# Kernel optimization log

Measured on AMD Instinct MI355X. Metric: run time of the kernel, lower is better.

Reference implementation:

```python
import jax, jax.numpy as jnp
import numpy as np
from jax import lax

B, H, W, CIN = 4, 64, 64, 1024
CMID = 512
NA = 9  # 3 sizes * 3 ratios
PRE_NMS, POST_NMS, IOU_THR = 6000, 300, 0.7  # eval-mode caps (training=False)


def setup_inputs() -> dict:
    key = jax.random.key(0)
    ks = jax.random.split(key, 4)
    feats = jax.random.normal(ks[0], (B, H, W, CIN), jnp.float32)
    # anchors: normalized ccwh (cx, cy, w, h) on a stride-16 grid of a 1024px image
    stride, img = 16.0, 1024.0
    cx = (jnp.arange(W, dtype=jnp.float32) + 0.5) * stride / img
    cy = (jnp.arange(H, dtype=jnp.float32) + 0.5) * stride / img
    sizes = jnp.array([64.0, 128.0, 256.0])
    ratios = jnp.array([0.5, 1.0, 2.0])
    ws = (sizes[:, None] * jnp.sqrt(ratios)[None, :]).reshape(-1) / img  # [9]
    hs = (sizes[:, None] / jnp.sqrt(ratios)[None, :]).reshape(-1) / img  # [9]
    cyg, cxg = jnp.meshgrid(cy, cx, indexing='ij')  # [H,W]
    ancs = jnp.stack([
        jnp.broadcast_to(cxg[:, :, None], (H, W, NA)),
        jnp.broadcast_to(cyg[:, :, None], (H, W, NA)),
        jnp.broadcast_to(ws[None, None, :], (H, W, NA)),
        jnp.broadcast_to(hs[None, None, :], (H, W, NA)),
    ], axis=-1)
    ancs = jnp.broadcast_to(ancs[None], (B, H, W, NA, 4)).astype(jnp.float32)
    ancs_valid = jnp.ones((B, H, W, NA), jnp.float32)
    w_bneck = jax.random.normal(ks[1], (CIN, CMID), jnp.float32) * 0.01
    b_bneck = jnp.zeros((CMID,), jnp.float32)
    w_cls = jax.random.normal(ks[2], (CMID, NA), jnp.float32) * 0.01
    b_cls = jnp.zeros((NA,), jnp.float32)
    w_reg = jax.random.normal(ks[3], (CMID, NA * 4), jnp.float32) * 0.01
    b_reg = jnp.zeros((NA * 4,), jnp.float32)
    return dict(feats=feats, ancs=ancs, ancs_valid=ancs_valid,
                w_bneck=w_bneck, b_bneck=b_bneck, w_cls=w_cls, b_cls=b_cls,
                w_reg=w_reg, b_reg=b_reg)


def _nms(boxes, max_out, thr):
    # boxes [N,4] xyxy, sorted by score descending. Greedy NMS via lax.scan.
    x1, y1, x2, y2 = boxes[:, 0], boxes[:, 1], boxes[:, 2], boxes[:, 3]
    areas = (x2 - x1) * (y2 - y1)

    def step(valid, _):
        idx = jnp.argmax(valid)  # first still-valid box = highest score
        has = valid[idx]
        b = boxes[idx]
        a = areas[idx]
        iw = jnp.maximum(jnp.minimum(b[2], x2) - jnp.maximum(b[0], x1), 0.0)
        ih = jnp.maximum(jnp.minimum(b[3], y2) - jnp.maximum(b[1], y1), 0.0)
        inter = iw * ih
        union = a + areas - inter
        iou = jnp.where(union > 0, inter / union, 0.0)
        keep = valid & (iou <= thr)
        keep = keep.at[idx].set(False)
        return jnp.where(has, keep, valid), jnp.where(has, idx, -1)

    _, sel = lax.scan(step, jnp.ones(boxes.shape[0], bool), None, length=max_out)
    return sel  # [max_out] selected indices, -1 = no more boxes


def _forward(feats, ancs, w_bneck, b_bneck, w_cls, b_cls, w_reg, b_reg):
    h = jax.nn.relu(jnp.einsum('bhwc,cm->bhwm', feats, w_bneck) + b_bneck)
    cls_pred = jax.nn.sigmoid(jnp.einsum('bhwm,mo->bhwo', h, w_cls) + b_cls)
    reg_pred = (jnp.einsum('bhwm,mo->bhwo', h, w_reg) + b_reg).reshape(B, H, W, NA, 4)
    cls_f = cls_pred.reshape(-1)
    reg_f = reg_pred.reshape(-1, 4)
    anc_f = ancs.reshape(-1, 4)
    # apply_offsets in ccwh: cx += tx*w, cy += ty*h, w *= exp(tw), h *= exp(th)
    cx = anc_f[:, 0] + reg_f[:, 0] * anc_f[:, 2]
    cy = anc_f[:, 1] + reg_f[:, 1] * anc_f[:, 3]
    ww = anc_f[:, 2] * jnp.exp(reg_f[:, 2])
    hh = anc_f[:, 3] * jnp.exp(reg_f[:, 3])
    # ccwh -> xyxy, clip to [0,1]
    boxes = jnp.stack([cx - ww / 2, cy - hh / 2, cx + ww / 2, cy + hh / 2], axis=-1)
    boxes = jnp.clip(boxes, 0.0, 1.0)
    order = jnp.argsort(-cls_f)[:PRE_NMS]
    boxes = boxes[order]
    sel = _nms(boxes, POST_NMS, IOU_THR)
    # pad unselected slots with zeros (TF returns a variable-length tensor)
    proposals = jnp.where(sel[:, None] >= 0, boxes[jnp.clip(sel, 0)], 0.0)
    return cls_pred, reg_pred, proposals


def reference(feats, ancs, ancs_valid, w_bneck, b_bneck, w_cls, b_cls, w_reg, b_reg):
    # ancs_valid is reshaped but never used in the original extract_proposals
    return _forward(feats, ancs, w_bneck, b_bneck, w_cls, b_cls, w_reg, b_reg)
```

## Files before the change

kernel.cpp:

```cpp
#include <hip/hip_runtime.h>
#include <cstdint>
#include <cstddef>

#define P_TOT    16384
#define CIN      1024
#define CMID     512
#define NA       9
#define NANC     147456
#define PRE_NMS  6000
#define POST_NMS 300
#define IOU_THR  0.7f
#define NWORDS   94
#define NHCOPY   64

#define CLS_OFF  0
#define REG_OFF  147456
#define PROP_OFF 737280

#define WS_H        0u
#define WS_MASK     0u
#define WS_HISTN    8388608u
#define WS_LOGITS   33554432u
#define WS_BOXES    36700160u
#define WS_HIST     39059456u
#define WS_WCOMB    39059456u
#define WS_META     39321600u
#define WS_COLL     39321856u
#define WS_SBOX     39387392u
#define CAP_COLL    8192

__device__ __forceinline__ int imin(int a, int b) { return a < b ? a : b; }

__device__ __forceinline__ void gld_lds16(const float* g, float* l) {
    __builtin_amdgcn_global_load_lds(
        (const __attribute__((address_space(1))) void*)g,
        (__attribute__((address_space(3))) void*)l,
        16, 0, 0);
}

__global__ __launch_bounds__(256) void gemm1_kernel(
    const float* __restrict__ A, const float* __restrict__ Bw,
    const float* __restrict__ bias, float* __restrict__ C)
{
    __shared__ float As[2][16][132];
    __shared__ float Bs[2][16][128];

    const int t  = threadIdx.x;
    const int m0 = blockIdx.x * 128;
    const int n0 = blockIdx.y * 128;
    const int tx = t & 15;
    const int ty = t >> 4;

    const int ar0 = t >> 2;
    const int ac0 = (t & 3) * 4;

    const float* asrc0 = A + (size_t)(m0 + ar0) * CIN + ac0;
    const float* asrc1 = asrc0 + (size_t)64 * CIN;
    const float* bsrc  = Bw + (size_t)(t >> 5) * CMID + n0 + (t & 31) * 4;
    float* bdst0 = &Bs[0][0][0] + t * 4;
    float* bdst1 = &Bs[1][0][0] + t * 4;

    float4 c0a{0,0,0,0}, c0b{0,0,0,0}, c1a{0,0,0,0}, c1b{0,0,0,0};
    float4 c2a{0,0,0,0}, c2b{0,0,0,0}, c3a{0,0,0,0}, c3b{0,0,0,0};
    float4 c4a{0,0,0,0}, c4b{0,0,0,0}, c5a{0,0,0,0}, c5b{0,0,0,0};
    float4 c6a{0,0,0,0}, c6b{0,0,0,0}, c7a{0,0,0,0}, c7b{0,0,0,0};

    gld_lds16(bsrc, bdst0);
    gld_lds16(bsrc + 8 * CMID, bdst0 + 1024);
    float4 pa0 = *(const float4*)(asrc0);
    float4 pa1 = *(const float4*)(asrc1);
    As[0][ac0 + 0][ar0] = pa0.x; As[0][ac0 + 1][ar0] = pa0.y;
    As[0][ac0 + 2][ar0] = pa0.z; As[0][ac0 + 3][ar0] = pa0.w;
    As[0][ac0 + 0][ar0 + 64] = pa1.x; As[0][ac0 + 1][ar0 + 64] = pa1.y;
    As[0][ac0 + 2][ar0 + 64] = pa1.z; As[0][ac0 + 3][ar0 + 64] = pa1.w;
    __syncthreads();

#define FMA4(acc, s, b) { acc.x += (s)*(b).x; acc.y += (s)*(b).y; \
                          acc.z += (s)*(b).z; acc.w += (s)*(b).w; }

    for (int kt = 0; kt < 64; ++kt) {
        const int cur = kt & 1, nxt = cur ^ 1;
        if (kt < 63) {
            const int k0 = (kt + 1) * 16;
            float* bd = nxt ? bdst1 : bdst0;
            gld_lds16(bsrc + (size_t)k0 * CMID, bd);
            gld_lds16(bsrc + (size_t)(k0 + 8) * CMID, bd + 1024);
            pa0 = *(const float4*)(asrc0 + k0);
            pa1 = *(const float4*)(asrc1 + k0);
        }
#pragma unroll 2
        for (int kk = 0; kk < 16; ++kk) {
            float4 a0 = *(const float4*)&As[cur][kk][ty * 4];
            float4 a1 = *(const float4*)&As[cur][kk][64 + ty * 4];
            float4 b0 = *(const float4*)&Bs[cur][kk][tx * 4];
            float4 b1 = *(const float4*)&Bs[cur][kk][64 + tx * 4];
            FMA4(c0a, a0.x, b0) FMA4(c0b, a0.x, b1)
            FMA4(c1a, a0.y, b0) FMA4(c1b, a0.y, b1)
            FMA4(c2a, a0.z, b0) FMA4(c2b, a0.z, b1)
            FMA4(c3a, a0.w, b0) FMA4(c3b, a0.w, b1)
            FMA4(c4a, a1.x, b0) FMA4(c4b, a1.x, b1)
            FMA4(c5a, a1.y, b0) FMA4(c5b, a1.y, b1)
            FMA4(c6a, a1.z, b0) FMA4(c6b, a1.z, b1)
            FMA4(c7a, a1.w, b0) FMA4(c7b, a1.w, b1)
        }
        if (kt < 63) {
            As[nxt][ac0 + 0][ar0] = pa0.x; As[nxt][ac0 + 1][ar0] = pa0.y;
            As[nxt][ac0 + 2][ar0] = pa0.z; As[nxt][ac0 + 3][ar0] = pa0.w;
            As[nxt][ac0 + 0][ar0 + 64] = pa1.x; As[nxt][ac0 + 1][ar0 + 64] = pa1.y;
            As[nxt][ac0 + 2][ar0 + 64] = pa1.z; As[nxt][ac0 + 3][ar0 + 64] = pa1.w;
        }
        __syncthreads();
    }
#undef FMA4

    const float4 bias0 = *(const float4*)(bias + n0 + tx * 4);
    const float4 bias1 = *(const float4*)(bias + n0 + 64 + tx * 4);
#define STROW(row, ca, cb) { \
    float4 o; \
    o.x = fmaxf(ca.x + bias0.x, 0.f); o.y = fmaxf(ca.y + bias0.y, 0.f); \
    o.z = fmaxf(ca.z + bias0.z, 0.f); o.w = fmaxf(ca.w + bias0.w, 0.f); \
    *(float4*)(C + (size_t)(row) * CMID + n0 + tx * 4) = o; \
    o.x = fmaxf(cb.x + bias1.x, 0.f); o.y = fmaxf(cb.y + bias1.y, 0.f); \
    o.z = fmaxf(cb.z + bias1.z, 0.f); o.w = fmaxf(cb.w + bias1.w, 0.f); \
    *(float4*)(C + (size_t)(row) * CMID + n0 + 64 + tx * 4) = o; }

    const int mr = m0 + ty * 4;
    STROW(mr + 0, c0a, c0b)   STROW(mr + 1, c1a, c1b)
    STROW(mr + 2, c2a, c2b)   STROW(mr + 3, c3a, c3b)
    STROW(mr + 64, c4a, c4b)  STROW(mr + 65, c5a, c5b)
    STROW(mr + 66, c6a, c6b)  STROW(mr + 67, c7a, c7b)
#undef STROW
}

__global__ __launch_bounds__(256) void wprep_kernel(
    const float* __restrict__ wcls, const float* __restrict__ wreg,
    float* __restrict__ wcomb)
{
    int i = blockIdx.x * 256 + threadIdx.x;
    int k = i / 48, o = i - k * 48;
    float v = 0.f;
    if (o < 9)       v = wcls[k * 9 + o];
    else if (o < 45) v = wreg[k * 36 + (o - 9)];
    wcomb[i] = v;
}

__global__ __launch_bounds__(256) void gemm2_kernel(
    const float* __restrict__ h, const float* __restrict__ wcomb,
    const float* __restrict__ bcls, const float* __restrict__ breg,
    float* __restrict__ logits)
{
    __shared__ float hS[64][33];
    __shared__ float wS[32][48];

    const int t  = threadIdx.x;
    const int p0 = blockIdx.x * 64;
    const int px = t & 63;
    const int og = t >> 6;

    const int hr = t >> 2;
    const int hc = (t & 3) * 4;

    float acc[12] = {};

    for (int kt = 0; kt < 16; ++kt) {
        const int k0 = kt * 32;
        {
            const float* hp = h + (size_t)(p0 + hr) * CMID + k0 + hc;
            float4 v0 = *(const float4*)(hp);
            float4 v1 = *(const float4*)(hp + 16);
            hS[hr][hc + 0] = v0.x; hS[hr][hc + 1] = v0.y;
            hS[hr][hc + 2] = v0.z; hS[hr][hc + 3] = v0.w;
            hS[hr][16 + hc + 0] = v1.x; hS[hr][16 + hc + 1] = v1.y;
            hS[hr][16 + hc + 2] = v1.z; hS[hr][16 + hc + 3] = v1.w;
        }
        {
            int idx = t;
            if (idx < 384) {
                int kk = idx / 12, o4 = (idx - kk * 12) * 4;
                *(float4*)&wS[kk][o4] = *(const float4*)&wcomb[(size_t)(k0 + kk) * 48 + o4];
            }
            idx = t + 256;
            if (idx < 384) {
                int kk = idx / 12, o4 = (idx - kk * 12) * 4;
                *(float4*)&wS[kk][o4] = *(const float4*)&wcomb[(size_t)(k0 + kk) * 48 + o4];
            }
        }
        __syncthreads();
#pragma unroll 4
        for (int kk = 0; kk < 32; ++kk) {
            float hv = hS[px][kk];
            float4 w0 = *(const float4*)&wS[kk][og * 12];
            float4 w1 = *(const float4*)&wS[kk][og * 12 + 4];
            float4 w2 = *(const float4*)&wS[kk][og * 12 + 8];
            acc[0] += hv * w0.x; acc[1]  += hv * w0.y; acc[2]  += hv * w0.z; acc[3]  += hv * w0.w;
            acc[4] += hv * w1.x; acc[5]  += hv * w1.y; acc[6]  += hv * w1.z; acc[7]  += hv * w1.w;
            acc[8] += hv * w2.x; acc[9]  += hv * w2.y; acc[10] += hv * w2.z; acc[11] += hv * w2.w;
        }
        __syncthreads();
    }
#pragma unroll
    for (int c = 0; c < 12; ++c) {
        int o = og * 12 + c;
        if (o < 45) {
            float bv = (o < 9) ? bcls[o] : breg[o - 9];
            logits[(size_t)(p0 + px) * 48 + o] = acc[c] + bv;
        }
    }
}

__global__ __launch_bounds__(256) void decode_kernel(
    const float* __restrict__ logits, const float4* __restrict__ ancs,
    float* __restrict__ out, float4* __restrict__ boxes,
    unsigned int* __restrict__ histN)
{
    int i = blockIdx.x * 256 + threadIdx.x;
    int p = i / 9, a = i - p * 9;
    const float* lrow = logits + (size_t)p * 48;
    float lg = lrow[a];
    float score = 1.f / (1.f + expf(-lg));
    out[CLS_OFF + i] = score;

    float r0 = lrow[9 + a * 4 + 0];
    float r1 = lrow[9 + a * 4 + 1];
    float r2 = lrow[9 + a * 4 + 2];
    float r3 = lrow[9 + a * 4 + 3];
    float4 rg; rg.x = r0; rg.y = r1; rg.z = r2; rg.w = r3;
    *(float4*)(out + REG_OFF + (size_t)i * 4) = rg;

    float4 an = ancs[i];
    float cx = an.x + r0 * an.z;
    float cy = an.y + r1 * an.w;
    float ww = an.z * expf(r2);
    float hh = an.w * expf(r3);
    float4 bb;
    bb.x = fminf(fmaxf(cx - ww * 0.5f, 0.f), 1.f);
    bb.y = fminf(fmaxf(cy - hh * 0.5f, 0.f), 1.f);
    bb.z = fminf(fmaxf(cx + ww * 0.5f, 0.f), 1.f);
    bb.w = fminf(fmaxf(cy + hh * 0.5f, 0.f), 1.f);
    boxes[i] = bb;

    unsigned int sb = __float_as_uint(score);
    atomicAdd(&histN[(unsigned)(blockIdx.x & (NHCOPY - 1)) * 65536u + (sb >> 16)], 1u);
}

__global__ __launch_bounds__(256) void hreduce_kernel(
    const unsigned int* __restrict__ histN, unsigned int* __restrict__ hist)
{
    int b = blockIdx.x * 256 + threadIdx.x;
    unsigned int s = 0;
#pragma unroll 8
    for (int c = 0; c < NHCOPY; ++c) s += histN[(unsigned)c * 65536u + b];
    hist[b] = s;
}

__global__ __launch_bounds__(256) void scan_kernel(
    const unsigned int* __restrict__ hist, unsigned int* __restrict__ meta)
{
    __shared__ unsigned int sums[256];
    __shared__ unsigned int sc[256];
    __shared__ unsigned int sc2[256];
    __shared__ int cstar;
    __shared__ unsigned int saShared;
    __shared__ int tbin;

    int t = threadIdx.x;
    if (t == 0) tbin = -1;

    unsigned int s = 0;
    int base = t << 8;
    for (int b = 0; b < 256; b += 4) {
        uint4 v = *(const uint4*)(hist + base + b);
        s += v.x + v.y + v.z + v.w;
    }
    sums[t] = s;
    __syncthreads();

    sc[t] = sums[255 - t];
    __syncthreads();
    for (int off = 1; off < 256; off <<= 1) {
        unsigned int v = sc[t];
        unsigned int add = (t >= off) ? sc[t - off] : 0u;
        __syncthreads();
        sc[t] = v + add;
        __syncthreads();
    }
    {
        unsigned int sa = (t == 255) ? 0u : sc[254 - t];
        if (sa < PRE_NMS && sa + sums[t] >= PRE_NMS) { cstar = t; saShared = sa; }
    }
    __syncthreads();

    int c = cstar;
    unsigned int SA = saShared;
    sc2[t] = hist[c * 256 + 255 - t];
    __syncthreads();
    for (int off = 1; off < 256; off <<= 1) {
        unsigned int v = sc2[t];
        unsigned int add = (t >= off) ? sc2[t - off] : 0u;
        __syncthreads();
        sc2[t] = v + add;
        __syncthreads();
    }
    {
        unsigned int si = sc2[255 - t];
        int cand = (SA + si >= PRE_NMS) ? t : -1;
        atomicMax(&tbin, cand);
    }
    __syncthreads();
    if (t == 0) meta[1] = (unsigned int)(c * 256 + tbin);
}

__global__ __launch_bounds__(256) void collect_kernel(
    const float* __restrict__ scores, const unsigned int* __restrict__ meta,
    unsigned long long* __restrict__ coll, unsigned int* __restrict__ cnt)
{
    int i = blockIdx.x * 256 + threadIdx.x;
    unsigned int T = meta[1];
    unsigned int sb = __float_as_uint(scores[i]);
    if ((sb >> 16) >= T) {
        unsigned int pos = atomicAdd(cnt, 1u);
        if (pos < CAP_COLL)
            coll[pos] = ((unsigned long long)sb << 32) |
                        (unsigned long long)(0xFFFFFFFFu - (unsigned int)i);
    }
}

__global__ __launch_bounds__(256) void rank_kernel(
    const unsigned long long* __restrict__ coll,
    const unsigned int* __restrict__ cnt,
    const float4* __restrict__ boxes, float4* __restrict__ sboxes)
{
    __shared__ unsigned long long ks[1024];
    const int t = threadIdx.x;
    const int gid = blockIdx.x * 256 + t;
    unsigned int n = cnt[0];
    if (n > CAP_COLL) n = CAP_COLL;
    unsigned long long me = (gid < (int)n) ? coll[gid] : 0ULL;
    int rank = 0;
    for (int base = 0; base < CAP_COLL; base += 1024) {
#pragma unroll
        for (int i = 0; i < 4; ++i) {
            int j = base + i * 256 + t;
            ks[i * 256 + t] = (j < (int)n) ? coll[j] : 0ULL;
        }
        __syncthreads();
#pragma unroll 8
        for (int j = 0; j < 1024; j += 2) {
            rank += (ks[j] > me) + (ks[j + 1] > me);
        }
        __syncthreads();
    }
    if (gid < (int)n && rank < PRE_NMS) {
        unsigned int idx = 0xFFFFFFFFu - (unsigned int)(me & 0xFFFFFFFFULL);
        if (idx > NANC - 1) idx = NANC - 1;
        sboxes[rank] = boxes[idx];
    }
}

__global__ __launch_bounds__(64) void nmsmat_kernel(
    const float4* __restrict__ sboxes, unsigned long long* __restrict__ mask)
{
    const int rb = blockIdx.x, cb = blockIdx.y;
    if (cb < rb) return;
    __shared__ float cx1[64], cy1[64], cx2[64], cy2[64], car[64];

    const int t = threadIdx.x;
    const int c = cb * 64 + t;
    float4 b = (c < PRE_NMS) ? sboxes[c] : make_float4(0.f, 0.f, 0.f, 0.f);
    cx1[t] = b.x; cy1[t] = b.y; cx2[t] = b.z; cy2[t] = b.w;
    car[t] = (b.z - b.x) * (b.w - b.y);
    __syncthreads();

    const int r = rb * 64 + t;
    if (r >= PRE_NMS) return;
    const float4 rbx = sboxes[r];
    const float ra = (rbx.z - rbx.x) * (rbx.w - rbx.y);

    unsigned long long w = 0ULL;
#pragma unroll 8
    for (int i = 0; i < 64; ++i) {
        int j = cb * 64 + i;
        float iw = fmaxf(fminf(rbx.z, cx2[i]) - fmaxf(rbx.x, cx1[i]), 0.f);
        float ih = fmaxf(fminf(rbx.w, cy2[i]) - fmaxf(rbx.y, cy1[i]), 0.f);
        float inter = iw * ih;
        float uni = ra + car[i] - inter;
        float iou = (uni > 0.f) ? (inter / uni) : 0.f;
        if (iou > IOU_THR && j > r) w |= (1ULL << i);
    }
    mask[(size_t)r * NWORDS + cb] = w;
}

__global__ __launch_bounds__(64) void nmsresolve_kernel(
    const float4* __restrict__ sboxes,
    const unsigned long long* __restrict__ mask,
    float* __restrict__ prop)
{
    const int t = threadIdx.x;
    for (int j = t; j < POST_NMS * 4; j += 64) prop[j] = 0.f;

    const int w0 = 2 * t, w1 = 2 * t + 1;
    unsigned long long v0 = 0ULL, v1 = 0ULL;
    if (w0 < 93) v0 = ~0ULL; else if (w0 == 93) v0 = (1ULL << 48) - 1ULL;
    if (w1 < 93) v1 = ~0ULL; else if (w1 == 93) v1 = (1ULL << 48) - 1ULL;

    int cnt = 0;
    while (cnt < POST_NMS) {
        int c = 0x7fffffff;
        if (v0) c = (w0 << 6) + __builtin_ctzll(v0);
        else if (v1) c = (w1 << 6) + __builtin_ctzll(v1);
        unsigned long long bal = __ballot((v0 | v1) != 0ULL);
        if (!bal) break;
        int F = __builtin_ctzll(bal);
        int g = __shfl(c, F, 64);
        const int wg = g >> 6, bg = g & 63;

        if (t == 0) {
            float4 bb = sboxes[g];
            *(float4*)(prop + cnt * 4) = bb;
        }
        const unsigned long long* row = mask + (size_t)g * NWORDS;
        unsigned long long m0 = (w0 >= wg) ? row[w0] : 0ULL;
        unsigned long long m1 = (w1 >= wg) ? row[w1] : 0ULL;
        v0 &= ~m0; v1 &= ~m1;
        if (w0 == wg) v0 &= ~(1ULL << bg);
        if (w1 == wg) v1 &= ~(1ULL << bg);
        ++cnt;
    }
}

extern "C" void kernel_launch(void* const* d_in, const int* in_sizes, int n_in,
                              void* d_out, int out_size, void* d_ws, size_t ws_size,
                              hipStream_t stream)
{
    const float*  feats   = (const float*)d_in[0];
    const float4* ancs    = (const float4*)d_in[1];
    const float*  w_bneck = (const float*)d_in[3];
    const float*  b_bneck = (const float*)d_in[4];
    const float*  w_cls   = (const float*)d_in[5];
    const float*  b_cls   = (const float*)d_in[6];
    const float*  w_reg   = (const float*)d_in[7];
    const float*  b_reg   = (const float*)d_in[8];

    float* out = (float*)d_out;
    char*  ws  = (char*)d_ws;
    float*              h      = (float*)(ws + WS_H);
    float*              logits = (float*)(ws + WS_LOGITS);
    float4*             boxes  = (float4*)(ws + WS_BOXES);
    unsigned int*       histN  = (unsigned int*)(ws + WS_HISTN);
    unsigned int*       hist   = (unsigned int*)(ws + WS_HIST);
    float*              wcomb  = (float*)(ws + WS_WCOMB);
    unsigned int*       meta   = (unsigned int*)(ws + WS_META);
    unsigned long long* coll   = (unsigned long long*)(ws + WS_COLL);
    float4*             sboxes = (float4*)(ws + WS_SBOX);
    unsigned long long* mask   = (unsigned long long*)(ws + WS_MASK);

    hipMemsetAsync(ws + WS_META, 0, 256, stream);

    wprep_kernel<<<96, 256, 0, stream>>>(w_cls, w_reg, wcomb);
    gemm1_kernel<<<dim3(128, 4), 256, 0, stream>>>(feats, w_bneck, b_bneck, h);
    gemm2_kernel<<<256, 256, 0, stream>>>(h, wcomb, b_cls, b_reg, logits);
    hipMemsetAsync(ws + WS_HISTN, 0, (size_t)NHCOPY * 65536 * 4, stream);
    decode_kernel<<<576, 256, 0, stream>>>(logits, ancs, out, boxes, histN);
    hreduce_kernel<<<256, 256, 0, stream>>>(histN, hist);
    scan_kernel<<<1, 256, 0, stream>>>(hist, meta);
    collect_kernel<<<576, 256, 0, stream>>>(out, meta, coll, &meta[0]);
    rank_kernel<<<32, 256, 0, stream>>>(coll, meta, boxes, sboxes);
    nmsmat_kernel<<<dim3(94, 94), 64, 0, stream>>>(sboxes, mask);
    nmsresolve_kernel<<<1, 64, 0, stream>>>(sboxes, mask, out + PROP_OFF);
}
```

Measured before the change: 718.7 us.

## Tune gemm1 occupancy, stream rank keys from global, vectorize NMS mask row loads

Adds a waves-per-EU hint to the bottleneck GEMM so the compiler can spend more registers per wave. The rank kernel drops its LDS staging and barriers: each thread reads the collected keys directly from global memory, and only up to the actual count rather than the fixed cap. The greedy NMS loop now loads each mask row as 16-byte pairs, with lanes below 47 fetching two adjacent words, instead of two separate 8-byte loads. Together these target register pressure, synchronisation and wasted comparisons, and NMS load latency on the serial critical path, at the cost of possibly lower occupancy in the GEMM. The NMS change assumes w0 and w1 are the adjacent pair 2t and 2t+1.

```diff
diff --git a/kernel.cpp b/kernel.cpp
--- a/kernel.cpp
+++ b/kernel.cpp
@@ -38,7 +38,9 @@
         16, 0, 0);
 }
 
-__global__ __launch_bounds__(256) void gemm1_kernel(
+__global__ __launch_bounds__(256)
+__attribute__((amdgpu_waves_per_eu(1, 2)))
+void gemm1_kernel(
     const float* __restrict__ A, const float* __restrict__ Bw,
     const float* __restrict__ bias, float* __restrict__ C)
 {
@@ -330,26 +332,23 @@
     const unsigned int* __restrict__ cnt,
     const float4* __restrict__ boxes, float4* __restrict__ sboxes)
 {
-    __shared__ unsigned long long ks[1024];
     const int t = threadIdx.x;
     const int gid = blockIdx.x * 256 + t;
     unsigned int n = cnt[0];
     if (n > CAP_COLL) n = CAP_COLL;
     unsigned long long me = (gid < (int)n) ? coll[gid] : 0ULL;
     int rank = 0;
-    for (int base = 0; base < CAP_COLL; base += 1024) {
-#pragma unroll
-        for (int i = 0; i < 4; ++i) {
-            int j = base + i * 256 + t;
-            ks[i * 256 + t] = (j < (int)n) ? coll[j] : 0ULL;
-        }
-        __syncthreads();
-#pragma unroll 8
-        for (int j = 0; j < 1024; j += 2) {
-            rank += (ks[j] > me) + (ks[j + 1] > me);
-        }
-        __syncthreads();
-    }
+    unsigned int j = 0;
+    for (; j + 8 <= n; j += 8) {
+        unsigned long long k0 = coll[j + 0], k1 = coll[j + 1];
+        unsigned long long k2 = coll[j + 2], k3 = coll[j + 3];
+        unsigned long long k4 = coll[j + 4], k5 = coll[j + 5];
+        unsigned long long k6 = coll[j + 6], k7 = coll[j + 7];
+        rank += (int)(k0 > me) + (int)(k1 > me) + (int)(k2 > me) + (int)(k3 > me)
+              + (int)(k4 > me) + (int)(k5 > me) + (int)(k6 > me) + (int)(k7 > me);
+    }
+    for (; j < n; ++j) rank += (int)(coll[j] > me);
+
     if (gid < (int)n && rank < PRE_NMS) {
         unsigned int idx = 0xFFFFFFFFu - (unsigned int)(me & 0xFFFFFFFFULL);
         if (idx > NANC - 1) idx = NANC - 1;
@@ -418,9 +417,14 @@
             float4 bb = sboxes[g];
             *(float4*)(prop + cnt * 4) = bb;
         }
-        const unsigned long long* row = mask + (size_t)g * NWORDS;
-        unsigned long long m0 = (w0 >= wg) ? row[w0] : 0ULL;
-        unsigned long long m1 = (w1 >= wg) ? row[w1] : 0ULL;
+        unsigned long long mx = 0ULL, my = 0ULL;
+        if (t < 47) {
+            const ulonglong2* row2 = (const ulonglong2*)(mask + (size_t)g * NWORDS);
+            ulonglong2 mm = row2[t];
+            mx = mm.x; my = mm.y;
+        }
+        unsigned long long m0 = (w0 >= wg) ? mx : 0ULL;
+        unsigned long long m1 = (w1 >= wg) ? my : 0ULL;
         v0 &= ~m0; v1 &= ~m1;
         if (w0 == wg) v0 &= ~(1ULL << bg);
         if (w1 == wg) v1 &= ~(1ULL << bg);
```

Result: slower. 866.0 us (+20.5%).
